# Kernel tuning notes

Hardware: AMD Instinct MI355X
Metric: run time of the kernel (lower is better)

The kernel has to match this reference:

```python
import jax, jax.numpy as jnp
import numpy as np
from jax.scipy.special import erf, erfinv

N = 1024
B = 262144
SQRT6 = float(np.sqrt(6.0))
SQRT3 = float(np.sqrt(3.0))


def setup_inputs() -> dict:
    key = jax.random.key(0)
    x = jax.random.normal(key, (B, 1), dtype=jnp.float32)
    centers = (jnp.arange(N, dtype=jnp.float32) / N + 1.0 / (2 * N))  # [N]
    return {"x": x, "centers": centers}


def _cdf_y(v):
    # CDF_Y(y) = 0.5*erf(sqrt(3)*erfinv(2y-1)) + 0.5
    return 0.5 * erf(SQRT3 * erfinv(2.0 * v - 1.0)) + 0.5


def reference(x, centers):
    n = centers.shape[0]
    # companding transform: y in (0,1), shape [B,1]
    y = 0.5 * erf(x / SQRT6) + 0.5
    # brute-force nearest-uniform-center search: [B,N]
    mse = (y - centers[None, :]) ** 2
    indices = jnp.argmin(mse, axis=1)            # [B] int
    y_hat = centers[indices][:, None]            # [B,1]
    x_hat = SQRT6 * erfinv(2.0 * y_hat - 1.0)    # [B,1]
    k = indices.astype(jnp.float32)
    likelihood = _cdf_y((k + 1.0) / n) - _cdf_y(k / n)  # [B]
    return (x_hat, likelihood, y_hat)
```

## Files before the change

### kernel.cpp

```cpp
#include <hip/hip_runtime.h>
#include <math.h>


#define B_ELEMS 262144
#define NC      1024

__device__ __forceinline__ void compand1(float x, float& xh, float& lik, float& yh) {
    const float INV_SQRT6 = 0.40824829046386302f;
    const float SQRT6     = 2.4494897427831781f;
    const float SQRT3     = 1.7320508075688772f;

    float y = 0.5f * erff(x * INV_SQRT6) + 0.5f;
    int k = (int)floorf(y * (float)NC);
    k = max(0, min(NC - 1, k));
    float kf = (float)k;

    yh = (kf + 0.5f) * (1.0f / (float)NC);
    xh = SQRT6 * erfinvf(2.0f * yh - 1.0f);

    float lo = (k == 0) ? 0.0f
             : fmaf(0.5f, erff(SQRT3 * erfinvf(fmaf(kf, 2.0f / (float)NC, -1.0f))), 0.5f);
    float hi = (k == NC - 1) ? 1.0f
             : fmaf(0.5f, erff(SQRT3 * erfinvf(fmaf(kf + 1.0f, 2.0f / (float)NC, -1.0f))), 0.5f);
    lik = hi - lo;
}

__global__ __launch_bounds__(256) void GaussianScalarCompander_kernel(
        const float* __restrict__ x, float* __restrict__ out) {
    int i = blockIdx.x * 256 + threadIdx.x;
    const float4* __restrict__ x4 = (const float4*)x;
    float4 xv = x4[i];

    float4 xh, lk, yh;
    compand1(xv.x, xh.x, lk.x, yh.x);
    compand1(xv.y, xh.y, lk.y, yh.y);
    compand1(xv.z, xh.z, lk.z, yh.z);
    compand1(xv.w, xh.w, lk.w, yh.w);

    float4* __restrict__ o_xh = (float4*)out;
    float4* __restrict__ o_lk = (float4*)(out + B_ELEMS);
    float4* __restrict__ o_yh = (float4*)(out + 2 * B_ELEMS);
    o_xh[i] = xh;
    o_lk[i] = lk;
    o_yh[i] = yh;
}

extern "C" void kernel_launch(void* const* d_in, const int* in_sizes, int n_in,
                              void* d_out, int out_size, void* d_ws, size_t ws_size,
                              hipStream_t stream) {
    const float* x = (const float*)d_in[0];
    float* out = (float*)d_out;

    const int n4 = B_ELEMS / 4;
    dim3 block(256);
    dim3 grid(n4 / 256);
    GaussianScalarCompander_kernel<<<grid, block, 0, stream>>>(x, out);
}
```

Baseline: 59.07 us.

## Precompute per-bin x_hat and likelihood tables, replace per-element erfinv with lookup

Adds a single-block kernel that computes the 1024 x_hat values and bin likelihoods once into workspace. The main kernel stages these tables in shared memory and indexes them per element, so each element needs one erf instead of three erfinv and two erf calls. It also switches from four elements per thread with float4 I/O to one scalar element per thread. The cost is an extra serial kernel launch, a table load per block, shared-memory gathers, and narrower memory accesses.

Measured after the change: 58.55 us. About the same (-0.9%).

```diff
diff --git a/kernel.cpp b/kernel.cpp
--- a/kernel.cpp
+++ b/kernel.cpp
@@ -5,44 +5,52 @@
 #define B_ELEMS 262144
 #define NC      1024
 
-__device__ __forceinline__ void compand1(float x, float& xh, float& lik, float& yh) {
-    const float INV_SQRT6 = 0.40824829046386302f;
-    const float SQRT6     = 2.4494897427831781f;
-    const float SQRT3     = 1.7320508075688772f;
+#define INV_SQRT6 0.40824829046386302f
+#define SQRT6     2.4494897427831781f
+#define SQRT3     1.7320508075688772f
 
-    float y = 0.5f * erff(x * INV_SQRT6) + 0.5f;
+__global__ __launch_bounds__(1024) void build_tables_kernel(
+        float* __restrict__ xh_tab, float* __restrict__ lik_tab) {
+    __shared__ float cdf[NC + 1];
+    const int k = threadIdx.x;
+
+    float c;
+    if (k == 0) {
+        c = 0.0f;
+    } else {
+        float v = (float)k * (1.0f / (float)NC);
+        c = fmaf(0.5f, erff(SQRT3 * erfinvf(fmaf(v, 2.0f, -1.0f))), 0.5f);
+    }
+    cdf[k] = c;
+    if (k == NC - 1) cdf[NC] = 1.0f;
+
+    float yh = ((float)k + 0.5f) * (1.0f / (float)NC);
+    xh_tab[k] = SQRT6 * erfinvf(fmaf(yh, 2.0f, -1.0f));
+
+    __syncthreads();
+    lik_tab[k] = cdf[k + 1] - cdf[k];
+}
+
+__global__ __launch_bounds__(256) void compand_kernel(
+        const float* __restrict__ x, float* __restrict__ out,
+        const float* __restrict__ xh_tab, const float* __restrict__ lik_tab) {
+    __shared__ float s_xh[NC];
+    __shared__ float s_lik[NC];
+    const int t = threadIdx.x;
+
+    ((float4*)s_xh)[t]  = ((const float4*)xh_tab)[t];
+    ((float4*)s_lik)[t] = ((const float4*)lik_tab)[t];
+    __syncthreads();
+
+    const int i = blockIdx.x * 256 + t;
+    float xv = x[i];
+    float y  = fmaf(0.5f, erff(xv * INV_SQRT6), 0.5f);
     int k = (int)floorf(y * (float)NC);
     k = max(0, min(NC - 1, k));
-    float kf = (float)k;
 
-    yh = (kf + 0.5f) * (1.0f / (float)NC);
-    xh = SQRT6 * erfinvf(2.0f * yh - 1.0f);
-
-    float lo = (k == 0) ? 0.0f
-             : fmaf(0.5f, erff(SQRT3 * erfinvf(fmaf(kf, 2.0f / (float)NC, -1.0f))), 0.5f);
-    float hi = (k == NC - 1) ? 1.0f
-             : fmaf(0.5f, erff(SQRT3 * erfinvf(fmaf(kf + 1.0f, 2.0f / (float)NC, -1.0f))), 0.5f);
-    lik = hi - lo;
-}
-
-__global__ __launch_bounds__(256) void GaussianScalarCompander_kernel(
-        const float* __restrict__ x, float* __restrict__ out) {
-    int i = blockIdx.x * 256 + threadIdx.x;
-    const float4* __restrict__ x4 = (const float4*)x;
-    float4 xv = x4[i];
-
-    float4 xh, lk, yh;
-    compand1(xv.x, xh.x, lk.x, yh.x);
-    compand1(xv.y, xh.y, lk.y, yh.y);
-    compand1(xv.z, xh.z, lk.z, yh.z);
-    compand1(xv.w, xh.w, lk.w, yh.w);
-
-    float4* __restrict__ o_xh = (float4*)out;
-    float4* __restrict__ o_lk = (float4*)(out + B_ELEMS);
-    float4* __restrict__ o_yh = (float4*)(out + 2 * B_ELEMS);
-    o_xh[i] = xh;
-    o_lk[i] = lk;
-    o_yh[i] = yh;
+    out[i]               = s_xh[k];
+    out[B_ELEMS + i]     = s_lik[k];
+    out[2 * B_ELEMS + i] = ((float)k + 0.5f) * (1.0f / (float)NC);
 }
 
 extern "C" void kernel_launch(void* const* d_in, const int* in_sizes, int n_in,
@@ -51,8 +59,12 @@
     const float* x = (const float*)d_in[0];
     float* out = (float*)d_out;
 
-    const int n4 = B_ELEMS / 4;
+    float* xh_tab  = (float*)d_ws;
+    float* lik_tab = (float*)d_ws + NC;
+
+    build_tables_kernel<<<1, NC, 0, stream>>>(xh_tab, lik_tab);
+
     dim3 block(256);
-    dim3 grid(n4 / 256);
-    GaussianScalarCompander_kernel<<<grid, block, 0, stream>>>(x, out);
+    dim3 grid(B_ELEMS / 256);
+    compand_kernel<<<grid, block, 0, stream>>>(x, out, xh_tab, lik_tab);
 }
```
